# Kernel tuning notes

Measured on AMD Instinct MI355X. Metric: run time of the kernel, lower is better.

The kernel has to match this reference:

```python
import jax, jax.numpy as jnp
import numpy as np

B, S, H, V = 32, 512, 768, 30522
N_UPDATE, MAX_LEN = 3, 8
NEG_INF = -1e9


def setup_inputs() -> dict:
    key = jax.random.key(0)
    ks = jax.random.split(key, 12)
    x = jax.random.randint(ks[0], (B, S), 0, V, dtype=jnp.int32)
    decoder_input = jax.random.normal(ks[1], (B, N_UPDATE, H), dtype=jnp.float32)
    encoder_output = jax.random.normal(ks[2], (B, S, H), dtype=jnp.float32)
    hidden = jax.random.normal(ks[3], (1, B, H), dtype=jnp.float32)
    teacher = jax.random.randint(ks[4], (B, N_UPDATE, MAX_LEN), 0, V, dtype=jnp.int32)
    # tied embedding table, padding_idx=0 row zeroed
    embed_w = (jax.random.normal(ks[5], (V, H), dtype=jnp.float32) * 0.02).at[0].set(0.0)
    # GRU weights ~ N(0, initializer_range=0.02), biases zero (torch default biases exist; keep small random)
    gru_w_ih = jax.random.normal(ks[6], (3 * H, H), dtype=jnp.float32) * 0.02
    gru_w_hh = jax.random.normal(ks[7], (3 * H, H), dtype=jnp.float32) * 0.02
    gru_b_ih = jax.random.normal(ks[8], (3 * H,), dtype=jnp.float32) * 0.02
    gru_b_hh = jax.random.normal(ks[9], (3 * H,), dtype=jnp.float32) * 0.02
    wgen_w = jax.random.normal(ks[10], (1, 3 * H), dtype=jnp.float32) * 0.02
    wgen_b = jnp.zeros((1,), dtype=jnp.float32)
    return {"x": x, "decoder_input": decoder_input, "encoder_output": encoder_output,
            "hidden": hidden, "teacher": teacher, "embed_w": embed_w,
            "gru_w_ih": gru_w_ih, "gru_w_hh": gru_w_hh, "gru_b_ih": gru_b_ih,
            "gru_b_hh": gru_b_hh, "wgen_w": wgen_w, "wgen_b": wgen_b, "max_len": MAX_LEN}


def _gru_cell(w, h, w_ih, w_hh, b_ih, b_hh):
    # PyTorch GRU cell. w, h: [B, H]
    gi = w @ w_ih.T + b_ih  # [B, 3H]
    gh = h @ w_hh.T + b_hh
    i_r, i_z, i_n = jnp.split(gi, 3, axis=-1)
    h_r, h_z, h_n = jnp.split(gh, 3, axis=-1)
    r = jax.nn.sigmoid(i_r + h_r)
    z = jax.nn.sigmoid(i_z + h_z)
    n = jnp.tanh(i_n + r * h_n)
    return (1.0 - z) * n + z * h


def reference(x, decoder_input, encoder_output, hidden, teacher, embed_w,
              gru_w_ih, gru_w_hh, gru_b_ih, gru_b_hh, wgen_w, wgen_b, max_len):
    b, n_update, hid = decoder_input.shape
    vocab = embed_w.shape[0]
    mask = (x == 0)  # [B, S]
    bidx = jnp.arange(b)[:, None]

    # Teacher-forced inputs: step 0 of slot j uses decoder_input[:, j];
    # step k>0 uses embed(teacher[:, j, k-1]).
    teacher_emb = embed_w[teacher]                     # [B, nU, L, H]
    inputs = jnp.concatenate([decoder_input[:, :, None, :], teacher_emb[:, :, :-1, :]], axis=2)
    inputs = inputs.transpose(1, 2, 0, 3).reshape(n_update * max_len, b, hid)  # [nU*L, B, H]

    h0 = hidden[0]  # [B, H]

    def step(h, w):
        h = _gru_cell(w, h, gru_w_ih, gru_w_hh, gru_b_ih, gru_b_hh)
        attn_e = jnp.einsum('bsh,bh->bs', encoder_output, h)
        attn_e = jnp.where(mask, NEG_INF, attn_e)
        attn_history = jax.nn.softmax(attn_e, axis=-1)          # [B, S]
        attn_vocab = jax.nn.softmax(h @ embed_w.T, axis=-1)     # [B, V]
        context = jnp.einsum('bs,bsh->bh', attn_history, encoder_output)
        p_gen = jax.nn.sigmoid(jnp.concatenate([w, h, context], axis=-1) @ wgen_w.T + wgen_b)  # [B,1]
        p_ctx = jnp.zeros((b, vocab), dtype=attn_vocab.dtype).at[bidx, x].add(attn_history)
        p_final = p_gen * attn_vocab + (1.0 - p_gen) * p_ctx    # [B, V]
        return h, p_final

    _, p_all = jax.lax.scan(step, h0, inputs)                    # [nU*L, B, V]
    p_all = p_all.reshape(n_update, max_len, b, vocab).transpose(2, 0, 1, 3)
    return p_all  # [B, n_update, max_len, V]
```

## Files before the change

kernel.cpp:

```cpp
#include <hip/hip_runtime.h>
#include <cstdint>

#define B_  32
#define S_  512
#define H_  768
#define V_  30522
#define NT_ 24
#define H3  2304
#define NC4   (V_*H_/4)
#define NWALL (NT_*B_*H_)
#define NINIT (B_*H_)

#define GRU_NBLK 192
#define GRU_TPB  512
#define GRU_JPB  4
#define GRU_RPB  12

typedef unsigned short ushort_t;
typedef __attribute__((ext_vector_type(8))) short bf16x8;
typedef __attribute__((ext_vector_type(4))) float f32x4;

__device__ __forceinline__ ushort_t f2bf(float f){
  union { float f; unsigned u; } v; v.f = f;
  unsigned r = v.u + 0x7fffu + ((v.u >> 16) & 1u);
  return (ushort_t)(r >> 16);
}

__device__ __forceinline__ void load_lds_16B(const void* g, void* l){
  auto gp = reinterpret_cast<const __attribute__((address_space(1))) unsigned int*>(
      reinterpret_cast<uintptr_t>(g));
  auto lp = reinterpret_cast<__attribute__((address_space(3))) unsigned int*>(
      reinterpret_cast<uintptr_t>(l));
  __builtin_amdgcn_global_load_lds(gp, lp, 16, 0, 0);
}

__global__ void k_prep(const float* __restrict__ embed, const float* __restrict__ dec,
                       const int* __restrict__ teacher, const float* __restrict__ hidden,
                       ushort_t* __restrict__ E2, float* __restrict__ wall,
                       float* __restrict__ Hq, float* __restrict__ Hb,
                       float* __restrict__ pgacc, unsigned* __restrict__ bar){
  int idx = blockIdx.x * 256 + threadIdx.x;
  if (idx < NC4){
    float4 v = ((const float4*)embed)[idx];
    uint2 o;
    o.x = (unsigned)f2bf(v.x) | ((unsigned)f2bf(v.y) << 16);
    o.y = (unsigned)f2bf(v.z) | ((unsigned)f2bf(v.w) << 16);
    ((uint2*)E2)[idx] = o;
    return;
  }
  idx -= NC4;
  if (idx < NWALL){
    int k  = idx % H_;
    int rb = idx / H_;
    int t = rb >> 5, b = rb & 31;
    int jj = t >> 3, kk = t & 7;
    float v;
    if (kk == 0) v = dec[(b*3 + jj)*H_ + k];
    else { int tok = teacher[(b*3 + jj)*8 + kk - 1]; v = embed[(size_t)tok*H_ + k]; }
    wall[idx] = v;
    return;
  }
  idx -= NWALL;
  if (idx < NINIT){
    int b = idx / H_, k = idx % H_;
    float v = hidden[idx];
    Hb[idx] = v;
    Hq[((k >> 1)*B_ + b)*2 + (k & 1)] = v;
    return;
  }
  idx -= NINIT;
  if (idx < 768){
    pgacc[idx] = 0.f;
    if (idx == 0) *bar = 0u;
  }
}

__global__ __launch_bounds__(256) void k_gi_gemm(const float* __restrict__ A, const float* __restrict__ Bm,
                                                 const float* __restrict__ bias, float* __restrict__ C){
  __shared__ float As[16][68];
  __shared__ float Bs[16][68];
  const int tid = threadIdx.x;
  const int tx = tid & 15, ty = tid >> 4;
  const int m0 = blockIdx.x * 64, n0 = blockIdx.y * 64;
  const int r = tid >> 2, kq = tid & 3;
  float acc[4][4] = {};
  for (int k0 = 0; k0 < 768; k0 += 16){
    float4 av = *(const float4*)&A [(size_t)(m0 + r)*768 + k0 + kq*4];
    float4 bv = *(const float4*)&Bm[(size_t)(n0 + r)*768 + k0 + kq*4];
    __syncthreads();
    As[kq*4+0][r] = av.x; As[kq*4+1][r] = av.y; As[kq*4+2][r] = av.z; As[kq*4+3][r] = av.w;
    Bs[kq*4+0][r] = bv.x; Bs[kq*4+1][r] = bv.y; Bs[kq*4+2][r] = bv.z; Bs[kq*4+3][r] = bv.w;
    __syncthreads();
#pragma unroll
    for (int kk = 0; kk < 16; ++kk){
      float4 a4 = *(const float4*)&As[kk][ty*4];
      float4 b4 = *(const float4*)&Bs[kk][tx*4];
      float aa[4] = {a4.x, a4.y, a4.z, a4.w};
      float bb[4] = {b4.x, b4.y, b4.z, b4.w};
#pragma unroll
      for (int i = 0; i < 4; ++i)
#pragma unroll
        for (int j = 0; j < 4; ++j)
          acc[i][j] = fmaf(aa[i], bb[j], acc[i][j]);
    }
  }
#pragma unroll
  for (int i = 0; i < 4; ++i){
    int m = m0 + ty*4 + i;
    int t = m >> 5, b = m & 31;
#pragma unroll
    for (int j = 0; j < 4; ++j){
      int n = n0 + tx*4 + j;
      C[((size_t)t*H3 + n)*32 + b] = acc[i][j] + bias[n];
    }
  }
}

__global__ __launch_bounds__(GRU_TPB) void k_gru_all(const float* __restrict__ gi, const float* __restrict__ whh,
                                                     const float* __restrict__ bhh, const float* __restrict__ hidden,
                                                     float* __restrict__ Hq, float* __restrict__ Hb,
                                                     ushort_t* __restrict__ A2, unsigned* __restrict__ bar){
  __shared__ float ws[GRU_RPB*768];
  __shared__ float red[16*392];
  __shared__ float bs[GRU_RPB];
  __shared__ float hn_st[128];
  const int tid = threadIdx.x;
  const int j0 = blockIdx.x * GRU_JPB;

  for (int idx4 = tid; idx4 < GRU_RPB*192; idx4 += GRU_TPB){
    int r = idx4 / 192, k4 = idx4 % 192;
    int gate = r >> 2, jl = r & 3;
    *(float4*)&ws[r*768 + k4*4] = *(const float4*)&whh[(size_t)(gate*768 + j0 + jl)*768 + k4*4];
  }
  if (tid < GRU_RPB) bs[tid] = bhh[(tid >> 2)*768 + j0 + (tid & 3)];
  __syncthreads();

  const int ks = tid >> 5, b = tid & 31;
  const int jl = tid >> 5, bb = tid & 31;
  const int j  = j0 + (jl & 3);
  float hp = 0.f;
  if (tid < 128) hp = hidden[bb*768 + j];

  for (int t = 0; t < NT_; ++t){
    const unsigned long long* hsrc = (const unsigned long long*)(Hq + (size_t)t*24576);

    float ir = 0.f, iz = 0.f, inn = 0.f;
    if (tid < 128){
      const float* gi_t = gi + (size_t)t*H3*32;
      ir  = gi_t[(size_t)(       j)*32 + bb];
      iz  = gi_t[(size_t)(768  + j)*32 + bb];
      inn = gi_t[(size_t)(1536 + j)*32 + bb];
    }

    float acc[GRU_RPB];
#pragma unroll
    for (int r = 0; r < GRU_RPB; ++r) acc[r] = 0.f;
#pragma unroll 8
    for (int i = 0; i < 24; ++i){
      union { unsigned long long u; float f[2]; } cv;
      cv.u = __hip_atomic_load(&hsrc[(size_t)(ks*24 + i)*32 + b],
                               __ATOMIC_RELAXED, __HIP_MEMORY_SCOPE_AGENT);
      const float h0 = cv.f[0], h1 = cv.f[1];
#pragma unroll
      for (int r = 0; r < GRU_RPB; ++r){
        const float2 w2 = *(const float2*)&ws[r*768 + ks*48 + i*2];
        acc[r] += h0*w2.x + h1*w2.y;
      }
    }
#pragma unroll
    for (int r = 0; r < GRU_RPB; ++r) red[ks*392 + r*32 + b] = acc[r];
    __syncthreads();

    if (tid < 128){
      float aR = 0.f, aZ = 0.f, aN = 0.f;
#pragma unroll
      for (int k8 = 0; k8 < 16; ++k8){
        aR += red[k8*392 + (0*GRU_JPB + jl)*32 + bb];
        aZ += red[k8*392 + (1*GRU_JPB + jl)*32 + bb];
        aN += red[k8*392 + (2*GRU_JPB + jl)*32 + bb];
      }
      aR += bs[jl]; aZ += bs[GRU_JPB + jl]; aN += bs[2*GRU_JPB + jl];
      float rg = 1.f / (1.f + __expf(-(ir + aR)));
      float zg = 1.f / (1.f + __expf(-(iz + aZ)));
      float e2 = __expf(-2.f*(inn + rg * aN));
      float ng = (1.f - e2) / (1.f + e2);
      float hn = (1.f - zg)*ng + zg*hp;
      hp = hn;
      Hb[(size_t)(t+1)*24576 + bb*768 + j] = hn;
      A2[(size_t)(t*32 + bb)*768 + j] = f2bf(hn);
      hn_st[jl*32 + bb] = hn;
    }
    __syncthreads();

    if (t < NT_ - 1){
      if (tid < 64){
        const int jp = tid >> 5, b2 = tid & 31;
        union { float f[2]; unsigned long long u; } cv;
        cv.f[0] = hn_st[(jp*2 + 0)*32 + b2];
        cv.f[1] = hn_st[(jp*2 + 1)*32 + b2];
        unsigned long long* hdst = (unsigned long long*)(Hq + (size_t)(t+1)*24576);
        __hip_atomic_store(&hdst[(size_t)(blockIdx.x*2 + jp)*32 + b2], cv.u,
                           __ATOMIC_RELAXED, __HIP_MEMORY_SCOPE_AGENT);
      }
      __syncthreads();
      if (tid == 0){
        __hip_atomic_fetch_add(bar, 1u, __ATOMIC_RELAXED, __HIP_MEMORY_SCOPE_AGENT);
        const unsigned tgt = (unsigned)(GRU_NBLK * (t + 1));
        unsigned spins = 0u;
        while (__hip_atomic_load(bar, __ATOMIC_RELAXED, __HIP_MEMORY_SCOPE_AGENT) < tgt &&
               ++spins < 20000000u)
          __builtin_amdgcn_s_sleep(2);
      }
      __syncthreads();
    }
  }
}

__global__ __launch_bounds__(256) void k_attn(const float* __restrict__ enc, const float* __restrict__ Hb1,
                                              float* __restrict__ ae){
  __shared__ float Es[64*36];
  __shared__ float Ht[24*36];
  const int b = blockIdx.x, s0 = blockIdx.y * 64;
  const int tid = threadIdx.x;
  const int s_l = tid & 63, tq = tid >> 6;
  const int r = tid >> 2, kq = tid & 3;
  float acc[6] = {0.f,0.f,0.f,0.f,0.f,0.f};
  for (int k0 = 0; k0 < 768; k0 += 32){
    __syncthreads();
    float4 e0 = *(const float4*)&enc[(size_t)(b*512 + s0 + r)*768 + k0 + kq*8];
    float4 e1 = *(const float4*)&enc[(size_t)(b*512 + s0 + r)*768 + k0 + kq*8 + 4];
    *(float4*)&Es[r*36 + kq*8]     = e0;
    *(float4*)&Es[r*36 + kq*8 + 4] = e1;
    if (tid < 192){
      int t = tid >> 3, k4 = tid & 7;
      *(float4*)&Ht[t*36 + k4*4] = *(const float4*)&Hb1[(size_t)t*24576 + b*768 + k0 + k4*4];
    }
    __syncthreads();
#pragma unroll
    for (int k4 = 0; k4 < 8; ++k4){
      float4 e = *(const float4*)&Es[s_l*36 + k4*4];
#pragma unroll
      for (int i = 0; i < 6; ++i){
        float4 h4 = *(const float4*)&Ht[(tq*6 + i)*36 + k4*4];
        acc[i] += e.x*h4.x + e.y*h4.y + e.z*h4.z + e.w*h4.w;
      }
    }
  }
#pragma unroll
  for (int i = 0; i < 6; ++i)
    ae[(size_t)((tq*6 + i)*32 + b)*512 + s0 + s_l] = acc[i];
}

__global__ __launch_bounds__(256) void k_attnsoft(const int* __restrict__ x, float* __restrict__ ae){
  const int row = blockIdx.x;
  const int b = row & 31;
  const int tid = threadIdx.x;
  __shared__ float red[256];
  float v0 = ae[(size_t)row*512 + tid];
  float v1 = ae[(size_t)row*512 + 256 + tid];
  if (x[b*512 + tid]        == 0) v0 = -1e9f;
  if (x[b*512 + 256 + tid]  == 0) v1 = -1e9f;
  float m = fmaxf(v0, v1);
  red[tid] = m; __syncthreads();
  for (int off = 128; off; off >>= 1){ if (tid < off) red[tid] = fmaxf(red[tid], red[tid+off]); __syncthreads(); }
  float M = red[0]; __syncthreads();
  float e0 = __expf(v0 - M), e1 = __expf(v1 - M);
  red[tid] = e0 + e1; __syncthreads();
  for (int off = 128; off; off >>= 1){ if (tid < off) red[tid] += red[tid+off]; __syncthreads(); }
  float inv = 1.f / red[0];
  ae[(size_t)row*512 + tid]       = e0 * inv;
  ae[(size_t)row*512 + 256 + tid] = e1 * inv;
}

__global__ __launch_bounds__(256) void k_ctx_pgen(const float* __restrict__ enc, const float* __restrict__ ah,
                                                  const float* __restrict__ wall, const float* __restrict__ Hb1,
                                                  const float* __restrict__ wg, float* __restrict__ pgacc){
  const int b = blockIdx.x;
  const int klane = threadIdx.x & 63;
  const int k = blockIdx.y * 64 + klane;
  const int tq = threadIdx.x >> 6;
  float acc[6] = {0.f,0.f,0.f,0.f,0.f,0.f};
  for (int s4 = 0; s4 < 512; s4 += 4){
    float e0 = enc[(size_t)(b*512 + s4 + 0)*768 + k];
    float e1 = enc[(size_t)(b*512 + s4 + 1)*768 + k];
    float e2 = enc[(size_t)(b*512 + s4 + 2)*768 + k];
    float e3 = enc[(size_t)(b*512 + s4 + 3)*768 + k];
#pragma unroll
    for (int i = 0; i < 6; ++i){
      float4 a4 = *(const float4*)&ah[(size_t)((tq*6 + i)*32 + b)*512 + s4];
      acc[i] = fmaf(a4.x, e0, acc[i]); acc[i] = fmaf(a4.y, e1, acc[i]);
      acc[i] = fmaf(a4.z, e2, acc[i]); acc[i] = fmaf(a4.w, e3, acc[i]);
    }
  }
  const float wgk = wg[k], wgh = wg[768 + k], wgc = wg[1536 + k];
#pragma unroll
  for (int i = 0; i < 6; ++i){
    const int t = tq*6 + i, row = t*32 + b;
    float p = acc[i]*wgc + wall[(size_t)row*768 + k]*wgk + Hb1[(size_t)t*24576 + b*768 + k]*wgh;
#pragma unroll
    for (int off = 32; off; off >>= 1) p += __shfl_down(p, off, 64);
    if (klane == 0) atomicAdd(&pgacc[row], p);
  }
}

__global__ __launch_bounds__(256) void k_vgemm(const ushort_t* __restrict__ A2, const ushort_t* __restrict__ E2,
                                               float* __restrict__ out){
  __shared__ ushort_t ldsA[128*64];
  __shared__ ushort_t ldsB[128*64];
  const int wg = blockIdx.x;
  const int xcd = wg & 7, qq = wg >> 3;
  const int ntile = (qq / 6) * 8 + xcd;
  const int mtile = qq % 6;
  const int tid = threadIdx.x;
  const int w = tid >> 6, lane = tid & 63;
  const int lrow = lane >> 3, lpos = lane & 7;
  const int wm = w >> 1, wn = w & 1;
  const int q = lane >> 4, fr = lane & 15;
  f32x4 acc[4][4];
  f32x4 zero = {0.f, 0.f, 0.f, 0.f};
#pragma unroll
  for (int a = 0; a < 4; ++a)
#pragma unroll
    for (int c = 0; c < 4; ++c) acc[a][c] = zero;

  for (int k0 = 0; k0 < 768; k0 += 64){
    __syncthreads();
#pragma unroll
    for (int i = 0; i < 4; ++i){
      int row = w*32 + i*8 + lrow;
      int c   = lpos ^ (row & 7);
      const ushort_t* srcA = A2 + (size_t)(mtile*128 + row)*768 + k0 + c*8;
      int brow = ntile*128 + row; if (brow > V_ - 1) brow = V_ - 1;
      const ushort_t* srcB = E2 + (size_t)brow*768 + k0 + c*8;
      load_lds_16B(srcA, &ldsA[row*64 + lpos*8]);
      load_lds_16B(srcB, &ldsB[row*64 + lpos*8]);
    }
    __builtin_amdgcn_s_waitcnt(0);
    __syncthreads();
#pragma unroll
    for (int s = 0; s < 2; ++s){
      bf16x8 af[4], bfr[4];
#pragma unroll
      for (int mt = 0; mt < 4; ++mt){
        int row = wm*64 + mt*16 + fr;
        int ch = (s*4 + q) ^ (row & 7);
        af[mt] = *(const bf16x8*)&ldsA[row*64 + ch*8];
      }
#pragma unroll
      for (int nt = 0; nt < 4; ++nt){
        int row = wn*64 + nt*16 + fr;
        int ch = (s*4 + q) ^ (row & 7);
        bfr[nt] = *(const bf16x8*)&ldsB[row*64 + ch*8];
      }
#pragma unroll
      for (int mt = 0; mt < 4; ++mt)
#pragma unroll
        for (int nt = 0; nt < 4; ++nt)
          acc[mt][nt] = __builtin_amdgcn_mfma_f32_16x16x32_bf16(af[mt], bfr[nt], acc[mt][nt], 0, 0, 0);
    }
  }
#pragma unroll
  for (int mt = 0; mt < 4; ++mt){
#pragma unroll
    for (int nt = 0; nt < 4; ++nt){
      int gn = ntile*128 + wn*64 + nt*16 + fr;
      if (gn >= V_) continue;
#pragma unroll
      for (int rg = 0; rg < 4; ++rg){
        int gm = mtile*128 + wm*64 + mt*16 + q*4 + rg;
        int t = gm >> 5, b = gm & 31;
        out[(size_t)(b*24 + t)*V_ + gn] = acc[mt][nt][rg];
      }
    }
  }
}

__global__ __launch_bounds__(512) void k_vsoft(float* __restrict__ out, const float* __restrict__ pgacc,
                                               const float* __restrict__ wgb){
  const int row = blockIdx.x;
  const int b = row / 24, t = row % 24;
  const float pg = 1.f / (1.f + __expf(-(pgacc[t*32 + b] + wgb[0])));
  const int tid = threadIdx.x;
  float* rp = out + (size_t)row * V_;
  const float4* rp4 = (const float4*)rp;
  float m = -3.0e38f, s = 0.f;
  for (int i = tid; i < 7630; i += 512){
    float4 v = rp4[i];
    float vm = fmaxf(fmaxf(v.x, v.y), fmaxf(v.z, v.w));
    float vs = __expf(v.x - vm) + __expf(v.y - vm) + __expf(v.z - vm) + __expf(v.w - vm);
    float nm = fmaxf(m, vm);
    s = s * __expf(m - nm) + vs * __expf(vm - nm);
    m = nm;
  }
  if (tid < 2){
    float v = rp[30520 + tid];
    float nm = fmaxf(m, v);
    s = s * __expf(m - nm) + __expf(v - nm);
    m = nm;
  }
#pragma unroll
  for (int off = 1; off < 64; off <<= 1){
    float m2 = __shfl_xor(m, off, 64), s2 = __shfl_xor(s, off, 64);
    float nm = fmaxf(m, m2);
    s = s*__expf(m - nm) + s2*__expf(m2 - nm);
    m = nm;
  }
  __shared__ float rm[8], rs[8];
  const int wid = tid >> 6;
  if ((tid & 63) == 0){ rm[wid] = m; rs[wid] = s; }
  __syncthreads();
  if (tid == 0){
    float M = rm[0], S = rs[0];
#pragma unroll
    for (int i = 1; i < 8; ++i){
      float m2 = rm[i], s2 = rs[i];
      float nm = fmaxf(M, m2);
      S = S*__expf(M - nm) + s2*__expf(m2 - nm);
      M = nm;
    }
    rm[0] = M; rs[0] = pg / S;
  }
  __syncthreads();
  const float M = rm[0], inv = rs[0];
  for (int i = tid; i < 7630; i += 512){
    float4 v = rp4[i];
    v.x = __expf(v.x - M) * inv;
    v.y = __expf(v.y - M) * inv;
    v.z = __expf(v.z - M) * inv;
    v.w = __expf(v.w - M) * inv;
    ((float4*)rp)[i] = v;
  }
  if (tid < 2) rp[30520 + tid] = __expf(rp[30520 + tid] - M) * inv;
}

__global__ void k_scatter(const float* __restrict__ ah, const float* __restrict__ pgacc,
                          const float* __restrict__ wgb, const int* __restrict__ x,
                          float* __restrict__ out){
  int idx = blockIdx.x * 256 + threadIdx.x;
  int s = idx & 511;
  int row = idx >> 9;
  int t = row >> 5, b = row & 31;
  float pg = 1.f / (1.f + __expf(-(pgacc[row] + wgb[0])));
  float val = ah[idx] * (1.f - pg);
  int col = x[b*512 + s];
  atomicAdd(&out[(size_t)(b*24 + t)*V_ + col], val);
}

extern "C" void kernel_launch(void* const* d_in, const int* in_sizes, int n_in,
                              void* d_out, int out_size, void* d_ws, size_t ws_size,
                              hipStream_t stream){
  (void)in_sizes; (void)n_in; (void)out_size; (void)ws_size;
  const int*   x      = (const int*)  d_in[0];
  const float* dec    = (const float*)d_in[1];
  const float* enc    = (const float*)d_in[2];
  const float* hidden = (const float*)d_in[3];
  const int*   teach  = (const int*)  d_in[4];
  const float* embed  = (const float*)d_in[5];
  const float* wih    = (const float*)d_in[6];
  const float* whh    = (const float*)d_in[7];
  const float* bih    = (const float*)d_in[8];
  const float* bhh    = (const float*)d_in[9];
  const float* wg     = (const float*)d_in[10];
  const float* wgb    = (const float*)d_in[11];
  float* out = (float*)d_out;

  char* p = (char*)d_ws;
  auto alloc = [&](size_t bytes){ void* r = (void*)p; p += (bytes + 255) & ~(size_t)255; return r; };
  ushort_t* E2  = (ushort_t*)alloc((size_t)V_ * H_ * 2);
  ushort_t* A2  = (ushort_t*)alloc((size_t)768 * 768 * 2);
  float* wall   = (float*)alloc((size_t)NT_ * B_ * H_ * 4);
  float* Hb     = (float*)alloc((size_t)(NT_+1) * B_ * H_ * 4);
  float* Hq     = (float*)alloc((size_t)(NT_+1) * B_ * H_ * 4);
  float* gi     = (float*)alloc((size_t)NT_ * B_ * H3 * 4);
  float* ae     = (float*)alloc((size_t)NT_ * B_ * S_ * 4);
  float* pgacc  = (float*)alloc(768 * 4);
  unsigned* bar = (unsigned*)alloc(256);

  const int prep_items  = NC4 + NWALL + NINIT + 768;
  const int prep_blocks = (prep_items + 255) / 256;

  k_prep<<<prep_blocks, 256, 0, stream>>>(embed, dec, teach, hidden, E2, wall, Hq, Hb, pgacc, bar);
  k_gi_gemm<<<dim3(12, 36), 256, 0, stream>>>(wall, wih, bih, gi);
  k_gru_all<<<GRU_NBLK, GRU_TPB, 0, stream>>>(gi, whh, bhh, hidden, Hq, Hb, A2, bar);
  k_attn<<<dim3(32, 8), 256, 0, stream>>>(enc, Hb + 24576, ae);
  k_attnsoft<<<768, 256, 0, stream>>>(x, ae);
  k_ctx_pgen<<<dim3(32, 12), 256, 0, stream>>>(enc, ae, wall, Hb + 24576, wg, pgacc);
  k_vgemm<<<1440, 256, 0, stream>>>(A2, E2, out);
  k_vsoft<<<768, 512, 0, stream>>>(out, pgacc, wgb);
  k_scatter<<<(NT_*B_*S_)/256, 256, 0, stream>>>(ae, pgacc, wgb, x, out);
}
```

Measured before the change: 823.1 us.

## Replace atomic counter grid barrier with per-block flags in GRU recurrence

```diff
diff --git a/kernel.cpp b/kernel.cpp
--- a/kernel.cpp
+++ b/kernel.cpp
@@ -38,7 +38,7 @@
                        const int* __restrict__ teacher, const float* __restrict__ hidden,
                        ushort_t* __restrict__ E2, float* __restrict__ wall,
                        float* __restrict__ Hq, float* __restrict__ Hb,
-                       float* __restrict__ pgacc, unsigned* __restrict__ bar){
+                       float* __restrict__ pgacc, unsigned* __restrict__ flags){
   int idx = blockIdx.x * 256 + threadIdx.x;
   if (idx < NC4){
     float4 v = ((const float4*)embed)[idx];
@@ -69,10 +69,9 @@
     return;
   }
   idx -= NINIT;
-  if (idx < 768){
-    pgacc[idx] = 0.f;
-    if (idx == 0) *bar = 0u;
-  }
+  if (idx < 768){ pgacc[idx] = 0.f; return; }
+  idx -= 768;
+  if (idx < 768) flags[idx] = 0u;
 }
 
 __global__ __launch_bounds__(256) void k_gi_gemm(const float* __restrict__ A, const float* __restrict__ Bm,
@@ -119,11 +118,10 @@
 __global__ __launch_bounds__(GRU_TPB) void k_gru_all(const float* __restrict__ gi, const float* __restrict__ whh,
                                                      const float* __restrict__ bhh, const float* __restrict__ hidden,
                                                      float* __restrict__ Hq, float* __restrict__ Hb,
-                                                     ushort_t* __restrict__ A2, unsigned* __restrict__ bar){
+                                                     ushort_t* __restrict__ A2, unsigned* __restrict__ flags){
   __shared__ float ws[GRU_RPB*768];
   __shared__ float red[16*392];
   __shared__ float bs[GRU_RPB];
-  __shared__ float hn_st[128];
   const int tid = threadIdx.x;
   const int j0 = blockIdx.x * GRU_JPB;
 
@@ -155,7 +153,7 @@
     float acc[GRU_RPB];
 #pragma unroll
     for (int r = 0; r < GRU_RPB; ++r) acc[r] = 0.f;
-#pragma unroll 8
+#pragma unroll
     for (int i = 0; i < 24; ++i){
       union { unsigned long long u; float f[2]; } cv;
       cv.u = __hip_atomic_load(&hsrc[(size_t)(ks*24 + i)*32 + b],
@@ -188,28 +186,25 @@
       hp = hn;
       Hb[(size_t)(t+1)*24576 + bb*768 + j] = hn;
       A2[(size_t)(t*32 + bb)*768 + j] = f2bf(hn);
-      hn_st[jl*32 + bb] = hn;
+      if (t < NT_ - 1){
+        union { float f; unsigned u; } hv; hv.f = hn;
+        unsigned* hq32 = (unsigned*)(Hq + (size_t)(t+1)*24576);
+        __hip_atomic_store(&hq32[((j >> 1)*32 + bb)*2 + (j & 1)], hv.u,
+                           __ATOMIC_RELAXED, __HIP_MEMORY_SCOPE_AGENT);
+      }
     }
     __syncthreads();
 
     if (t < NT_ - 1){
-      if (tid < 64){
-        const int jp = tid >> 5, b2 = tid & 31;
-        union { float f[2]; unsigned long long u; } cv;
-        cv.f[0] = hn_st[(jp*2 + 0)*32 + b2];
-        cv.f[1] = hn_st[(jp*2 + 1)*32 + b2];
-        unsigned long long* hdst = (unsigned long long*)(Hq + (size_t)(t+1)*24576);
-        __hip_atomic_store(&hdst[(size_t)(blockIdx.x*2 + jp)*32 + b2], cv.u,
+      if (tid == 0)
+        __hip_atomic_store(&flags[(size_t)blockIdx.x*4], (unsigned)(t + 1),
                            __ATOMIC_RELAXED, __HIP_MEMORY_SCOPE_AGENT);
-      }
-      __syncthreads();
-      if (tid == 0){
-        __hip_atomic_fetch_add(bar, 1u, __ATOMIC_RELAXED, __HIP_MEMORY_SCOPE_AGENT);
-        const unsigned tgt = (unsigned)(GRU_NBLK * (t + 1));
+      if (tid < GRU_NBLK){
         unsigned spins = 0u;
-        while (__hip_atomic_load(bar, __ATOMIC_RELAXED, __HIP_MEMORY_SCOPE_AGENT) < tgt &&
+        while (__hip_atomic_load(&flags[(size_t)tid*4], __ATOMIC_RELAXED,
+                                 __HIP_MEMORY_SCOPE_AGENT) < (unsigned)(t + 1) &&
                ++spins < 20000000u)
-          __builtin_amdgcn_s_sleep(2);
+          __builtin_amdgcn_s_sleep(1);
       }
       __syncthreads();
     }
@@ -474,14 +469,14 @@
   float* gi     = (float*)alloc((size_t)NT_ * B_ * H3 * 4);
   float* ae     = (float*)alloc((size_t)NT_ * B_ * S_ * 4);
   float* pgacc  = (float*)alloc(768 * 4);
-  unsigned* bar = (unsigned*)alloc(256);
-
-  const int prep_items  = NC4 + NWALL + NINIT + 768;
+  unsigned* flags = (unsigned*)alloc(768 * 4);
+
+  const int prep_items  = NC4 + NWALL + NINIT + 768 + 768;
   const int prep_blocks = (prep_items + 255) / 256;
 
-  k_prep<<<prep_blocks, 256, 0, stream>>>(embed, dec, teach, hidden, E2, wall, Hq, Hb, pgacc, bar);
+  k_prep<<<prep_blocks, 256, 0, stream>>>(embed, dec, teach, hidden, E2, wall, Hq, Hb, pgacc, flags);
   k_gi_gemm<<<dim3(12, 36), 256, 0, stream>>>(wall, wih, bih, gi);
-  k_gru_all<<<GRU_NBLK, GRU_TPB, 0, stream>>>(gi, whh, bhh, hidden, Hq, Hb, A2, bar);
+  k_gru_all<<<GRU_NBLK, GRU_TPB, 0, stream>>>(gi, whh, bhh, hidden, Hq, Hb, A2, flags);
   k_attn<<<dim3(32, 8), 256, 0, stream>>>(enc, Hb + 24576, ae);
   k_attnsoft<<<768, 256, 0, stream>>>(x, ae);
   k_ctx_pgen<<<dim3(32, 12), 256, 0, stream>>>(enc, ae, wall, Hb + 24576, wg, pgacc);
```

After: 731.2 us. 11.2% less time.
